# Kernel optimization log

Measured on AMD Instinct MI355X. Metric: run time of the kernel, lower is better.

Reference implementation:

```python
import jax, jax.numpy as jnp
import numpy as np

N = 4_194_304          # number of rays
DAMPING = 0.5          # LM(0.5)
MAX_DELTA = 1000.0     # clamp on LM step
N_ITER = 30            # no_grad warmup iterations
XMIN, XMAX, TAU = -1.0, 1.0, 1.0


def _surface_F(pts, c):
    # implicit parabolic rod: F(p) = x - c*(y^2 + z^2); pts: [N,3]
    return pts[..., 0] - c * (pts[..., 1] ** 2 + pts[..., 2] ** 2)


def _lm_delta(P, V, t, c):
    # Levenberg-Marquardt step for f(t) = F(P + t*V):
    # delta = f * f' / (f'^2 + damping), clamped to [-max_delta, max_delta]
    pts = P + t[:, None] * V                     # [N,3]
    f = _surface_F(pts, c)                       # [N]
    # f'(t) = gradF(pts) . V, gradF = (1, -2c*y, -2c*z)
    fp = V[:, 0] - 2.0 * c * (pts[:, 1] * V[:, 1] + pts[:, 2] * V[:, 2])
    delta = f * fp / (fp * fp + DAMPING)
    return jnp.clip(delta, -MAX_DELTA, MAX_DELTA)


def setup_inputs() -> dict:
    key = jax.random.key(0)
    k1, k2 = jax.random.split(key, 2)
    P = jax.random.normal(k1, (N, 3), jnp.float32) * 2.0
    V = jax.random.normal(k2, (N, 3), jnp.float32)
    V = V / jnp.linalg.norm(V, axis=-1, keepdims=True)
    a, b = 0.3, -0.2
    Rz = jnp.array([[np.cos(a), -np.sin(a), 0.0],
                    [np.sin(a),  np.cos(a), 0.0],
                    [0.0,        0.0,       1.0]], jnp.float32)
    Ry = jnp.array([[np.cos(b), 0.0, np.sin(b)],
                    [0.0,       1.0, 0.0],
                    [-np.sin(b), 0.0, np.cos(b)]], jnp.float32)
    R = Rz @ Ry                                  # rigid rotation [3,3]
    T = jnp.array([0.1, -0.2, 0.05], jnp.float32)
    c = jnp.float32(0.05)
    loss_in = jnp.float32(0.0)
    return {"P": P, "V": V, "R": R, "T": T, "c": c, "loss_in": loss_in}


def reference(P, V, R, T, c, loss_in):
    n = P.shape[0]
    # transform.inverse_points / inverse_vectors: R^T (p - T), R^T v
    P_local = (P - T) @ R                        # [N,3]
    V_local = V @ R                              # [N,3]

    # 30 no-grad LM iterations (torch.no_grad -> stop_gradient on inputs)
    Pl = jax.lax.stop_gradient(P_local)
    Vl = jax.lax.stop_gradient(V_local)
    cs = jax.lax.stop_gradient(c)

    def body(i, t):
        return t - _lm_delta(Pl, Vl, t, cs)

    t0 = jax.lax.fori_loop(0, N_ITER, body, jnp.zeros((n,), jnp.float32))

    # final differentiable LM step
    t = t0 - _lm_delta(P_local, V_local, t0, c)

    points_local = P_local + t[:, None] * V_local
    scale = jnp.mean(jnp.abs(jnp.array([XMIN, XMAX, TAU], jnp.float32)))
    F = _surface_F(points_local, c) / scale
    loss = loss_in + jnp.sum(F ** 2) / n
    return loss
```

## Files before the change

kernel.cpp:

```cpp
#include <hip/hip_runtime.h>


#define LM_ITERS 31
constexpr float DAMPING = 0.5f;

__global__ __launch_bounds__(256) void rod_kernel(
    const float* __restrict__ P, const float* __restrict__ V,
    const float* __restrict__ Rm, const float* __restrict__ Tv,
    const float* __restrict__ c_ptr, double* __restrict__ ws, int n)
{
    const float c  = c_ptr[0];
    const float r00 = Rm[0], r01 = Rm[1], r02 = Rm[2];
    const float r10 = Rm[3], r11 = Rm[4], r12 = Rm[5];
    const float r20 = Rm[6], r21 = Rm[7], r22 = Rm[8];
    const float t0 = Tv[0], t1 = Tv[1], t2 = Tv[2];

    const int tid  = blockIdx.x * blockDim.x + threadIdx.x;
    const int base = tid * 4;

    double acc = 0.0;
    if (base < n) {
        const float4* P4 = (const float4*)P;
        const float4* V4 = (const float4*)V;
        float4 pa = P4[tid * 3 + 0], pb = P4[tid * 3 + 1], pcv = P4[tid * 3 + 2];
        float4 va = V4[tid * 3 + 0], vb = V4[tid * 3 + 1], vcv = V4[tid * 3 + 2];

        const float px[4] = {pa.x, pa.w, pb.z, pcv.y};
        const float py[4] = {pa.y, pb.x, pb.w, pcv.z};
        const float pz[4] = {pa.z, pb.y, pcv.x, pcv.w};
        const float vx[4] = {va.x, va.w, vb.z, vcv.y};
        const float vy[4] = {va.y, vb.x, vb.w, vcv.z};
        const float vz[4] = {va.z, vb.y, vcv.x, vcv.w};

        float nA[4], f[4], fp[4];
        #pragma unroll
        for (int r = 0; r < 4; ++r) {
            const float qx = px[r] - t0, qy = py[r] - t1, qz = pz[r] - t2;
            const float plx = qx * r00 + qy * r10 + qz * r20;
            const float ply = qx * r01 + qy * r11 + qz * r21;
            const float plz = qx * r02 + qy * r12 + qz * r22;
            const float vlx = vx[r] * r00 + vy[r] * r10 + vz[r] * r20;
            const float vly = vx[r] * r01 + vy[r] * r11 + vz[r] * r21;
            const float vlz = vx[r] * r02 + vy[r] * r12 + vz[r] * r22;
            nA[r] = c * (vly * vly + vlz * vlz);
            f[r]  = plx - c * (ply * ply + plz * plz);
            fp[r] = vlx - 2.0f * c * (ply * vly + plz * vlz);
        }

        #pragma unroll 1
        for (int it = 0; it < LM_ITERS; ++it) {
            #pragma unroll
            for (int r = 0; r < 4; ++r) {
                const float den = fmaf(fp[r], fp[r], DAMPING);
                const float rcp = __builtin_amdgcn_rcpf(den);
                const float d   = (f[r] * fp[r]) * rcp;
                const float tmp = fmaf(nA[r], d, fp[r]);
                f[r]  = fmaf(-d, tmp, f[r]);
                fp[r] = fmaf(nA[r], d, tmp);
            }
        }

        #pragma unroll
        for (int r = 0; r < 4; ++r) {
            if (base + r < n)
                acc += (double)f[r] * (double)f[r];
        }
    }

    for (int off = 32; off > 0; off >>= 1)
        acc += __shfl_down(acc, off, 64);
    __shared__ double sacc[4];
    const int lane = threadIdx.x & 63, wave = threadIdx.x >> 6;
    if (lane == 0) sacc[wave] = acc;
    __syncthreads();
    if (threadIdx.x == 0) {
        atomicAdd(ws, sacc[0] + sacc[1] + sacc[2] + sacc[3]);
    }
}

__global__ void rod_finalize(const double* __restrict__ ws,
                             const float* __restrict__ loss_in,
                             float* __restrict__ out, double inv_n)
{
    out[0] = (float)(ws[0] * inv_n + (double)loss_in[0]);
}

extern "C" void kernel_launch(void* const* d_in, const int* in_sizes, int n_in,
                              void* d_out, int out_size, void* d_ws, size_t ws_size,
                              hipStream_t stream) {
    const float* P       = (const float*)d_in[0];
    const float* V       = (const float*)d_in[1];
    const float* R       = (const float*)d_in[2];
    const float* T       = (const float*)d_in[3];
    const float* c       = (const float*)d_in[4];
    const float* loss_in = (const float*)d_in[5];

    const int n = in_sizes[0] / 3;

    hipMemsetAsync(d_ws, 0, sizeof(double), stream);

    const int threads = (n + 3) / 4;
    const int block   = 256;
    const int grid    = (threads + block - 1) / block;
    rod_kernel<<<grid, block, 0, stream>>>(P, V, R, T, c, (double*)d_ws, n);
    rod_finalize<<<1, 1, 0, stream>>>((const double*)d_ws, loss_in,
                                      (float*)d_out, 1.0 / (double)n);
}
```

Measured before the change: 160.9 us.

## Process two ray groups per thread, prefetching second group's loads during first compute

Each thread now handles two groups of four rays, strided by the grid size, and halves the launch grid. The second group's P and V loads are issued before the first group's LM iterations run, so their memory latency overlaps with compute. This also halves the number of blocks and atomics. The cost is more registers held live per thread, which may lower occupancy, and fewer waves available to hide latency.

```diff
diff --git a/kernel.cpp b/kernel.cpp
--- a/kernel.cpp
+++ b/kernel.cpp
@@ -15,38 +15,48 @@
     const float r20 = Rm[6], r21 = Rm[7], r22 = Rm[8];
     const float t0 = Tv[0], t1 = Tv[1], t2 = Tv[2];
 
-    const int tid  = blockIdx.x * blockDim.x + threadIdx.x;
-    const int base = tid * 4;
+    const int tid      = blockIdx.x * blockDim.x + threadIdx.x;
+    const int nthreads = gridDim.x * blockDim.x;
+    const int g0 = tid;
+    const int g1 = tid + nthreads;
+
+    const float4* P4 = (const float4*)P;
+    const float4* V4 = (const float4*)V;
 
     double acc = 0.0;
-    if (base < n) {
-        const float4* P4 = (const float4*)P;
-        const float4* V4 = (const float4*)V;
-        float4 pa = P4[tid * 3 + 0], pb = P4[tid * 3 + 1], pcv = P4[tid * 3 + 2];
-        float4 va = V4[tid * 3 + 0], vb = V4[tid * 3 + 1], vcv = V4[tid * 3 + 2];
 
-        const float px[4] = {pa.x, pa.w, pb.z, pcv.y};
-        const float py[4] = {pa.y, pb.x, pb.w, pcv.z};
-        const float pz[4] = {pa.z, pb.y, pcv.x, pcv.w};
-        const float vx[4] = {va.x, va.w, vb.z, vcv.y};
-        const float vy[4] = {va.y, vb.x, vb.w, vcv.z};
-        const float vz[4] = {va.z, vb.y, vcv.x, vcv.w};
+    float4 pa{}, pb{}, pcv{}, va{}, vb{}, vcv{};
+    const bool has0 = (4 * g0 < n);
+    if (has0) {
+        pa = P4[g0 * 3 + 0]; pb = P4[g0 * 3 + 1]; pcv = P4[g0 * 3 + 2];
+        va = V4[g0 * 3 + 0]; vb = V4[g0 * 3 + 1]; vcv = V4[g0 * 3 + 2];
+    }
 
-        float nA[4], f[4], fp[4];
+    float nA[4], f[4], fp[4];
+    auto setup4 = [&](const float4& qa, const float4& qb, const float4& qc,
+                      const float4& ua, const float4& ub, const float4& uc) {
+        const float px[4] = {qa.x, qa.w, qb.z, qc.y};
+        const float py[4] = {qa.y, qb.x, qb.w, qc.z};
+        const float pz[4] = {qa.z, qb.y, qc.x, qc.w};
+        const float wx[4] = {ua.x, ua.w, ub.z, uc.y};
+        const float wy[4] = {ua.y, ub.x, ub.w, uc.z};
+        const float wz[4] = {ua.z, ub.y, uc.x, uc.w};
         #pragma unroll
         for (int r = 0; r < 4; ++r) {
             const float qx = px[r] - t0, qy = py[r] - t1, qz = pz[r] - t2;
             const float plx = qx * r00 + qy * r10 + qz * r20;
             const float ply = qx * r01 + qy * r11 + qz * r21;
             const float plz = qx * r02 + qy * r12 + qz * r22;
-            const float vlx = vx[r] * r00 + vy[r] * r10 + vz[r] * r20;
-            const float vly = vx[r] * r01 + vy[r] * r11 + vz[r] * r21;
-            const float vlz = vx[r] * r02 + vy[r] * r12 + vz[r] * r22;
+            const float vlx = wx[r] * r00 + wy[r] * r10 + wz[r] * r20;
+            const float vly = wx[r] * r01 + wy[r] * r11 + wz[r] * r21;
+            const float vlz = wx[r] * r02 + wy[r] * r12 + wz[r] * r22;
             nA[r] = c * (vly * vly + vlz * vlz);
             f[r]  = plx - c * (ply * ply + plz * plz);
             fp[r] = vlx - 2.0f * c * (ply * vly + plz * vlz);
         }
+    };
 
+    auto iterate = [&]() {
         #pragma unroll 1
         for (int it = 0; it < LM_ITERS; ++it) {
             #pragma unroll
@@ -59,12 +69,30 @@
                 fp[r] = fmaf(nA[r], d, tmp);
             }
         }
+    };
 
+    setup4(pa, pb, pcv, va, vb, vcv);
+
+    float4 qa1{}, qb1{}, qc1{}, ua1{}, ub1{}, uc1{};
+    const bool has1 = (4 * g1 < n);
+    if (has1) {
+        qa1 = P4[g1 * 3 + 0]; qb1 = P4[g1 * 3 + 1]; qc1 = P4[g1 * 3 + 2];
+        ua1 = V4[g1 * 3 + 0]; ub1 = V4[g1 * 3 + 1]; uc1 = V4[g1 * 3 + 2];
+    }
+
+    iterate();
+    if (has0) {
         #pragma unroll
-        for (int r = 0; r < 4; ++r) {
-            if (base + r < n)
-                acc += (double)f[r] * (double)f[r];
-        }
+        for (int r = 0; r < 4; ++r)
+            if (4 * g0 + r < n) acc += (double)f[r] * (double)f[r];
+    }
+
+    setup4(qa1, qb1, qc1, ua1, ub1, uc1);
+    iterate();
+    if (has1) {
+        #pragma unroll
+        for (int r = 0; r < 4; ++r)
+            if (4 * g1 + r < n) acc += (double)f[r] * (double)f[r];
     }
 
     for (int off = 32; off > 0; off >>= 1)
@@ -99,7 +127,7 @@
 
     hipMemsetAsync(d_ws, 0, sizeof(double), stream);
 
-    const int threads = (n + 3) / 4;
+    const int threads = (n + 7) / 8;
     const int block   = 256;
     const int grid    = (threads + block - 1) / block;
     rod_kernel<<<grid, block, 0, stream>>>(P, V, R, T, c, (double*)d_ws, n);
```

Measured after the change: 144.3 us. -10.3%, faster.
